# Kernel optimization log

Measured on AMD Instinct MI355X. Metric: run time of the kernel, lower is better.

The kernel has to match this reference:

```python
import jax, jax.numpy as jnp
import numpy as np

C = 512
H = 8

def setup_inputs() -> dict:
    key = jax.random.key(0)
    ks = jax.random.split(key, 5)
    x = jax.random.normal(ks[0], (4, C, 2048), dtype=jnp.float32)
    # Conv1d(kernel_size=1) == pointwise linear: weight [out, in], bias [out]
    qkv_w = jax.random.normal(ks[1], (3 * C, C), dtype=jnp.float32) * (1.0 / np.sqrt(C))
    qkv_b = jax.random.normal(ks[2], (3 * C,), dtype=jnp.float32) * 0.02
    proj_w = jax.random.normal(ks[3], (C, C), dtype=jnp.float32) * (1.0 / np.sqrt(C))
    proj_b = jax.random.normal(ks[4], (C,), dtype=jnp.float32) * 0.02
    return {"x": x, "qkv_w": qkv_w, "qkv_b": qkv_b, "proj_w": proj_w, "proj_b": proj_b}

def reference(x, qkv_w, qkv_b, proj_w, proj_b):
    b, c, t = x.shape
    scale = c ** (-0.5)  # NOTE: full channel count, matching the torch module
    # pointwise conv: [3C, C] @ [b, C, T] -> [b, 3C, T]
    qkv = jnp.einsum('oc,bct->bot', qkv_w, x) + qkv_b[None, :, None]
    q, k, v = jnp.split(qkv, 3, axis=1)
    d = c // H
    q = q.reshape(b, H, d, t)
    k = k.reshape(b, H, d, t)
    v = v.reshape(b, H, d, t)
    attn = jnp.einsum('bhct,bhcs->bhts', q, k) * scale
    attn = jax.nn.softmax(attn, axis=-1)
    out = jnp.einsum('bhts,bhcs->bhct', attn, v)
    out = out.reshape(b, c, t)
    out = jnp.einsum('oc,bct->bot', proj_w, out) + proj_b[None, :, None]
    return x + out
```

## Files before the change

### kernel.cpp

```cpp
#include <hip/hip_runtime.h>
#include <hip/hip_bf16.h>
#include <math.h>

#define B_DIM 4
#define C_DIM 512
#define T_DIM 2048
#define H_DIM 8
#define OC3   1536
#define VN_STRIDE 2064
#define SCALE 0.044194173824159216f
#define SCALE2 (0.044194173824159216f * 1.4426950408889634f)

typedef unsigned short ushortT;
typedef unsigned int uintT;
typedef __attribute__((ext_vector_type(8))) short bf16x8;
typedef __attribute__((ext_vector_type(4))) short bf16x4;
typedef __attribute__((ext_vector_type(4))) float f32x4;

__device__ __forceinline__ ushortT f2bf(float f) {
    union { float f; uintT u; } v; v.f = f;
    uintT r = v.u + 0x7FFF + ((v.u >> 16) & 1);
    return (ushortT)(r >> 16);
}
__device__ __forceinline__ float bf2f(ushortT h) {
    union { uintT u; float f; } v; v.u = ((uintT)h) << 16;
    return v.f;
}
__device__ __forceinline__ uintT pack2bf(float a, float b) {
    uintT ua = __float_as_uint(a) + 0x8000u;
    uintT ub = __float_as_uint(b) + 0x8000u;
    return (ua >> 16) | (ub & 0xFFFF0000u);
}
__device__ __forceinline__ uintT cvtpk2bf(float a, float b) {
    union { __bf16 v[2]; uintT u; } c;
    c.v[0] = (__bf16)a; c.v[1] = (__bf16)b;
    return c.u;
}
__device__ __forceinline__ void gload_lds16(const ushortT* g, ushortT* l) {
    __builtin_amdgcn_global_load_lds(
        (const __attribute__((address_space(1))) void*)g,
        (__attribute__((address_space(3))) void*)l, 16, 0, 0);
}

__global__ __launch_bounds__(256) void prep(const float* __restrict__ x,
                                            const float* __restrict__ qw,
                                            const float* __restrict__ pw,
                                            ushortT* __restrict__ xb,
                                            ushortT* __restrict__ qwb,
                                            ushortT* __restrict__ pwb) {
    __shared__ float xs[64][65];
    const int tid = threadIdx.x;
    const int blk = blockIdx.x;
    if (blk >= 1024) {
        int idx = ((blk - 1024) * 256 + tid) * 4;
        if (idx < OC3 * C_DIM) {
            float4 v = *(const float4*)(qw + idx);
            qwb[idx + 0] = f2bf(v.x); qwb[idx + 1] = f2bf(v.y);
            qwb[idx + 2] = f2bf(v.z); qwb[idx + 3] = f2bf(v.w);
        } else {
            idx -= OC3 * C_DIM;
            float4 v = *(const float4*)(pw + idx);
            pwb[idx + 0] = f2bf(v.x); pwb[idx + 1] = f2bf(v.y);
            pwb[idx + 2] = f2bf(v.z); pwb[idx + 3] = f2bf(v.w);
        }
        return;
    }
    const int b = blk >> 8, rem = blk & 255;
    const int c0 = (rem >> 5) * 64, t0 = (rem & 31) * 64;
    #pragma unroll
    for (int it = 0; it < 4; ++it) {
        int idx = it * 256 + tid;
        int r = idx >> 4, ch = idx & 15;
        float4 v = *(const float4*)(x + ((size_t)(b * C_DIM + c0 + r)) * T_DIM + t0 + ch * 4);
        xs[r][ch * 4 + 0] = v.x; xs[r][ch * 4 + 1] = v.y;
        xs[r][ch * 4 + 2] = v.z; xs[r][ch * 4 + 3] = v.w;
    }
    __syncthreads();
    #pragma unroll
    for (int it = 0; it < 2; ++it) {
        int idx = it * 256 + tid;
        int rt = idx >> 3, ch = idx & 7;
        union { ushortT s[8]; uint4 v; } tmp;
        #pragma unroll
        for (int k = 0; k < 8; ++k) tmp.s[k] = f2bf(xs[ch * 8 + k][rt]);
        *(uint4*)(xb + ((size_t)b * T_DIM + t0 + rt) * C_DIM + c0 + ch * 8) = tmp.v;
    }
}

__global__ __launch_bounds__(256, 2) void gemm_qkv(const ushortT* __restrict__ A,
                                                   const ushortT* __restrict__ Bw,
                                                   const float* __restrict__ bias,
                                                   ushortT* __restrict__ out,
                                                   ushortT* __restrict__ Vn) {
    __shared__ __align__(16) ushortT As[8192], Bs[8192];
    const int tid = threadIdx.x, lane = tid & 63, wid = tid >> 6;
    const int u = lane & 15, q = lane >> 4;
    const int wm = wid & 1, wn = wid >> 1;
    const int m0 = blockIdx.x * 128, n0 = blockIdx.y * 128;
    const int lrow = lane >> 2, lcol = (lane & 3) * 8;

    f32x4 acc[4][4];
    const f32x4 z = {0.f, 0.f, 0.f, 0.f};
    #pragma unroll
    for (int mi = 0; mi < 4; ++mi)
        #pragma unroll
        for (int ni = 0; ni < 4; ++ni) acc[mi][ni] = z;

    for (int k0 = 0; k0 < 512; k0 += 64) {
        __syncthreads();
        gload_lds16(A  + (size_t)(m0 + wid * 32 +      lrow) * 512 + k0      + lcol, &As[(wid * 32     ) * 32]);
        gload_lds16(A  + (size_t)(m0 + wid * 32 + 16 + lrow) * 512 + k0      + lcol, &As[(wid * 32 + 16) * 32]);
        gload_lds16(A  + (size_t)(m0 + wid * 32 +      lrow) * 512 + k0 + 32 + lcol, &As[4096 + (wid * 32     ) * 32]);
        gload_lds16(A  + (size_t)(m0 + wid * 32 + 16 + lrow) * 512 + k0 + 32 + lcol, &As[4096 + (wid * 32 + 16) * 32]);
        gload_lds16(Bw + (size_t)(n0 + wid * 32 +      lrow) * 512 + k0      + lcol, &Bs[(wid * 32     ) * 32]);
        gload_lds16(Bw + (size_t)(n0 + wid * 32 + 16 + lrow) * 512 + k0      + lcol, &Bs[(wid * 32 + 16) * 32]);
        gload_lds16(Bw + (size_t)(n0 + wid * 32 +      lrow) * 512 + k0 + 32 + lcol, &Bs[4096 + (wid * 32     ) * 32]);
        gload_lds16(Bw + (size_t)(n0 + wid * 32 + 16 + lrow) * 512 + k0 + 32 + lcol, &Bs[4096 + (wid * 32 + 16) * 32]);
        __syncthreads();
        bf16x8 af[4][2], bfr[4][2];
        #pragma unroll
        for (int mi = 0; mi < 4; ++mi) {
            af[mi][0] = *(const bf16x8*)&As[(wm * 64 + mi * 16 + u) * 32 + q * 8];
            af[mi][1] = *(const bf16x8*)&As[4096 + (wm * 64 + mi * 16 + u) * 32 + q * 8];
        }
        #pragma unroll
        for (int ni = 0; ni < 4; ++ni) {
            bfr[ni][0] = *(const bf16x8*)&Bs[(wn * 64 + ni * 16 + u) * 32 + q * 8];
            bfr[ni][1] = *(const bf16x8*)&Bs[4096 + (wn * 64 + ni * 16 + u) * 32 + q * 8];
        }
        #pragma unroll
        for (int mi = 0; mi < 4; ++mi)
            #pragma unroll
            for (int ni = 0; ni < 4; ++ni) {
                acc[mi][ni] = __builtin_amdgcn_mfma_f32_16x16x32_bf16(
                    af[mi][0], bfr[ni][0], acc[mi][ni], 0, 0, 0);
                acc[mi][ni] = __builtin_amdgcn_mfma_f32_16x16x32_bf16(
                    af[mi][1], bfr[ni][1], acc[mi][ni], 0, 0, 0);
            }
    }
    if (n0 < 1024) {
        const float scl = (n0 < 512) ? SCALE2 : 1.0f;
        #pragma unroll
        for (int ni = 0; ni < 4; ++ni) {
            int o = n0 + wn * 64 + ni * 16 + u;
            float bv = bias[o];
            #pragma unroll
            for (int mi = 0; mi < 4; ++mi)
                #pragma unroll
                for (int r = 0; r < 4; ++r) {
                    int m = m0 + wm * 64 + mi * 16 + q * 4 + r;
                    out[(size_t)m * OC3 + o] = f2bf((acc[mi][ni][r] + bv) * scl);
                }
        }
    } else {
        #pragma unroll
        for (int ni = 0; ni < 4; ++ni) {
            int o = n0 + wn * 64 + ni * 16 + u;
            float bv = bias[o];
            int oo = o - 1024;
            int hv = oo >> 6, d = oo & 63;
            #pragma unroll
            for (int mi = 0; mi < 4; ++mi) {
                int m = m0 + wm * 64 + mi * 16 + q * 4;
                int b = m >> 11, t = m & 2047;
                uint2 w;
                w.x = pack2bf(acc[mi][ni][0] + bv, acc[mi][ni][1] + bv);
                w.y = pack2bf(acc[mi][ni][2] + bv, acc[mi][ni][3] + bv);
                *(uint2*)(Vn + ((size_t)((b * 8 + hv) * 64 + d)) * VN_STRIDE + t) = w;
            }
        }
    }
}

__global__ __launch_bounds__(256, 2)
void flash(const ushortT* __restrict__ qkvT, const ushortT* __restrict__ Vn,
           ushortT* __restrict__ AO)
{
    __shared__ __align__(16) ushortT smem[16384];

    const int tid = threadIdx.x, lane = tid & 63, wid = tid >> 6;
    const int u = lane & 15, q = lane >> 4;
    const int g = blockIdx.x;
    const int bh = (g & 7) * 4 + ((g >> 3) & 3);
    const int qt = g >> 5;
    const int bb = bh >> 3, h = bh & 7;
    const int q0 = qt * 128;
    const size_t qbase = (size_t)bb * T_DIM * OC3;

    bf16x8 qb[2][2];
    #pragma unroll
    for (int ti = 0; ti < 2; ++ti)
        #pragma unroll
        for (int kst = 0; kst < 2; ++kst)
            qb[ti][kst] = *(const bf16x8*)(qkvT + qbase
                + (size_t)(q0 + wid * 32 + ti * 16 + u) * OC3 + h * 64 + kst * 32 + q * 8);

    const int rs = wid * 8 + (lane >> 3);
    const int sg = (lane & 7) ^ (rs & 7);
    const ushortT* ks0 = qkvT + qbase + (size_t)(rs     ) * OC3 + 512 + h * 64 + sg * 8;
    const ushortT* ks1 = qkvT + qbase + (size_t)(rs + 32) * OC3 + 512 + h * 64 + sg * 8;
    const ushortT* vs0 = Vn + ((size_t)bh * 64 + rs     ) * VN_STRIDE + sg * 8;
    const ushortT* vs1 = Vn + ((size_t)bh * 64 + rs + 32) * VN_STRIDE + sg * 8;

    f32x4 acc[4][2];
    const f32x4 z = {0.f, 0.f, 0.f, 0.f};
    #pragma unroll
    for (int ci = 0; ci < 4; ++ci)
        #pragma unroll
        for (int ti = 0; ti < 2; ++ti) acc[ci][ti] = z;
    f32x4 lacc[2] = {z, z};
    const bf16x4 ones = {(short)0x3F80, (short)0x3F80, (short)0x3F80, (short)0x3F80};

    gload_lds16(ks0, &smem[       wid * 512]);
    gload_lds16(ks1, &smem[2048 + wid * 512]);
    gload_lds16(vs0, &smem[8192 +        wid * 512]);
    gload_lds16(vs1, &smem[8192 + 2048 + wid * 512]);
    ks0 += 64 * OC3; ks1 += 64 * OC3; vs0 += 64; vs1 += 64;
    __syncthreads();

    int cur = 0;
    for (int rnd = 0; rnd < 32; ++rnd) {
        if (rnd < 31) {
            int nb = cur ^ 1;
            gload_lds16(ks0, &smem[nb * 4096 +        wid * 512]);
            gload_lds16(ks1, &smem[nb * 4096 + 2048 + wid * 512]);
            gload_lds16(vs0, &smem[8192 + nb * 4096 +        wid * 512]);
            gload_lds16(vs1, &smem[8192 + nb * 4096 + 2048 + wid * 512]);
            ks0 += 64 * OC3; ks1 += 64 * OC3; vs0 += 64; vs1 += 64;
        }
        const ushortT* Kb = &smem[cur * 4096];
        const ushortT* Vb = &smem[8192 + cur * 4096];
        bf16x8 ka[4][2];
        #pragma unroll
        for (int si = 0; si < 4; ++si)
            #pragma unroll
            for (int kst = 0; kst < 2; ++kst)
                ka[si][kst] = *(const bf16x8*)&Kb[(si * 16 + u) * 64
                    + (((kst * 4 + q) ^ (u & 7)) * 8)];
        bf16x4 va[4][4];
        #pragma unroll
        for (int si = 0; si < 4; ++si)
            #pragma unroll
            for (int ci = 0; ci < 4; ++ci)
                va[si][ci] = *(const bf16x4*)&Vb[(ci * 16 + u) * 64
                    + (((si * 2 + (q >> 1)) ^ (u & 7)) * 8) + (q & 1) * 4];

        #pragma unroll
        for (int si = 0; si < 4; ++si) {
            f32x4 sacc[2] = {z, z};
            #pragma unroll
            for (int ti = 0; ti < 2; ++ti)
                sacc[ti] = __builtin_amdgcn_mfma_f32_16x16x32_bf16(
                    ka[si][0], qb[ti][0], sacc[ti], 0, 0, 0);
            #pragma unroll
            for (int ti = 0; ti < 2; ++ti)
                sacc[ti] = __builtin_amdgcn_mfma_f32_16x16x32_bf16(
                    ka[si][1], qb[ti][1], sacc[ti], 0, 0, 0);
            #pragma unroll
            for (int ti = 0; ti < 2; ++ti) {
                float p0 = __builtin_amdgcn_exp2f(sacc[ti][0]);
                float p1 = __builtin_amdgcn_exp2f(sacc[ti][1]);
                float p2 = __builtin_amdgcn_exp2f(sacc[ti][2]);
                float p3 = __builtin_amdgcn_exp2f(sacc[ti][3]);
                union { uint2 u2; bf16x4 v; } pw;
                pw.u2.x = cvtpk2bf(p0, p1);
                pw.u2.y = cvtpk2bf(p2, p3);
                lacc[ti] = __builtin_amdgcn_mfma_f32_16x16x16bf16_1k(
                    ones, pw.v, lacc[ti], 0, 0, 0);
                #pragma unroll
                for (int ci = 0; ci < 4; ++ci)
                    acc[ci][ti] = __builtin_amdgcn_mfma_f32_16x16x16bf16_1k(
                        va[si][ci], pw.v, acc[ci][ti], 0, 0, 0);
            }
        }
        __syncthreads();
        cur ^= 1;
    }

    ushortT* Ob = smem + wid * 2304;
    float* Lb = (float*)(smem + 9216);
    if (q == 0) {
        Lb[wid * 32 + u]      = lacc[0][0];
        Lb[wid * 32 + 16 + u] = lacc[1][0];
    }
    #pragma unroll
    for (int ci = 0; ci < 4; ++ci)
        #pragma unroll
        for (int ti = 0; ti < 2; ++ti) {
            uint2 w;
            w.x = pack2bf(acc[ci][ti][0], acc[ci][ti][1]);
            w.y = pack2bf(acc[ci][ti][2], acc[ci][ti][3]);
            *(uint2*)&Ob[(ti * 16 + u) * 72 + ci * 16 + q * 4] = w;
        }
    __syncthreads();
    {
        const int row = tid >> 1, cs = (tid & 1) * 32;
        const int w = row >> 5, r32 = row & 31;
        float linv = 1.0f / Lb[w * 32 + r32];
        const ushortT* rp = smem + w * 2304 + r32 * 72 + cs;
        size_t orow = ((size_t)bb * T_DIM + q0 + row) * C_DIM + h * 64 + cs;
        #pragma unroll
        for (int j = 0; j < 4; ++j) {
            uint4 rv = *(const uint4*)(rp + j * 8);
            const uintT* rpp = (const uintT*)&rv;
            uint4 o;
            uintT* op = (uintT*)&o;
            #pragma unroll
            for (int k = 0; k < 4; ++k)
                op[k] = pack2bf(bf2f((ushortT)(rpp[k] & 0xFFFF)) * linv,
                                bf2f((ushortT)(rpp[k] >> 16)) * linv);
            *(uint4*)(AO + orow + j * 8) = o;
        }
    }
}

__global__ __launch_bounds__(256, 2) void gemm_proj(const ushortT* __restrict__ Wp,
                                                    const ushortT* __restrict__ AOv,
                                                    const float* __restrict__ bias,
                                                    const float* __restrict__ xres,
                                                    float* __restrict__ out) {
    __shared__ __align__(16) ushortT As[8192], Bs[8192];
    const int tid = threadIdx.x, lane = tid & 63, wid = tid >> 6;
    const int u = lane & 15, q = lane >> 4;
    const int wm = wid & 1, wn = wid >> 1;
    const int m0 = blockIdx.y * 128, n0 = blockIdx.x * 128;
    const int lrow = lane >> 2, lcol = (lane & 3) * 8;

    f32x4 acc[4][4];
    const f32x4 z = {0.f, 0.f, 0.f, 0.f};
    #pragma unroll
    for (int mi = 0; mi < 4; ++mi)
        #pragma unroll
        for (int ni = 0; ni < 4; ++ni) acc[mi][ni] = z;

    for (int k0 = 0; k0 < 512; k0 += 64) {
        __syncthreads();
        gload_lds16(Wp  + (size_t)(m0 + wid * 32 +      lrow) * 512 + k0      + lcol, &As[(wid * 32     ) * 32]);
        gload_lds16(Wp  + (size_t)(m0 + wid * 32 + 16 + lrow) * 512 + k0      + lcol, &As[(wid * 32 + 16) * 32]);
        gload_lds16(Wp  + (size_t)(m0 + wid * 32 +      lrow) * 512 + k0 + 32 + lcol, &As[4096 + (wid * 32     ) * 32]);
        gload_lds16(Wp  + (size_t)(m0 + wid * 32 + 16 + lrow) * 512 + k0 + 32 + lcol, &As[4096 + (wid * 32 + 16) * 32]);
        gload_lds16(AOv + (size_t)(n0 + wid * 32 +      lrow) * 512 + k0      + lcol, &Bs[(wid * 32     ) * 32]);
        gload_lds16(AOv + (size_t)(n0 + wid * 32 + 16 + lrow) * 512 + k0      + lcol, &Bs[(wid * 32 + 16) * 32]);
        gload_lds16(AOv + (size_t)(n0 + wid * 32 +      lrow) * 512 + k0 + 32 + lcol, &Bs[4096 + (wid * 32     ) * 32]);
        gload_lds16(AOv + (size_t)(n0 + wid * 32 + 16 + lrow) * 512 + k0 + 32 + lcol, &Bs[4096 + (wid * 32 + 16) * 32]);
        __syncthreads();
        bf16x8 af[4][2], bfr[4][2];
        #pragma unroll
        for (int mi = 0; mi < 4; ++mi) {
            af[mi][0] = *(const bf16x8*)&As[(wm * 64 + mi * 16 + u) * 32 + q * 8];
            af[mi][1] = *(const bf16x8*)&As[4096 + (wm * 64 + mi * 16 + u) * 32 + q * 8];
        }
        #pragma unroll
        for (int ni = 0; ni < 4; ++ni) {
            bfr[ni][0] = *(const bf16x8*)&Bs[(wn * 64 + ni * 16 + u) * 32 + q * 8];
            bfr[ni][1] = *(const bf16x8*)&Bs[4096 + (wn * 64 + ni * 16 + u) * 32 + q * 8];
        }
        #pragma unroll
        for (int mi = 0; mi < 4; ++mi)
            #pragma unroll
            for (int ni = 0; ni < 4; ++ni) {
                acc[mi][ni] = __builtin_amdgcn_mfma_f32_16x16x32_bf16(
                    af[mi][0], bfr[ni][0], acc[mi][ni], 0, 0, 0);
                acc[mi][ni] = __builtin_amdgcn_mfma_f32_16x16x32_bf16(
                    af[mi][1], bfr[ni][1], acc[mi][ni], 0, 0, 0);
            }
    }
    #pragma unroll
    for (int mi = 0; mi < 4; ++mi)
        #pragma unroll
        for (int r = 0; r < 4; ++r) {
            int o = m0 + wm * 64 + mi * 16 + q * 4 + r;
            float bv = bias[o];
            #pragma unroll
            for (int ni = 0; ni < 4; ++ni) {
                int n = n0 + wn * 64 + ni * 16 + u;
                int b = n >> 11, t = n & 2047;
                size_t oi = ((size_t)b * C_DIM + o) * T_DIM + t;
                out[oi] = acc[mi][ni][r] + bv + xres[oi];
            }
        }
}

extern "C" void kernel_launch(void* const* d_in, const int* in_sizes, int n_in,
                              void* d_out, int out_size, void* d_ws, size_t ws_size,
                              hipStream_t stream)
{
    const float* x      = (const float*)d_in[0];
    const float* qkv_w  = (const float*)d_in[1];
    const float* qkv_b  = (const float*)d_in[2];
    const float* proj_w = (const float*)d_in[3];
    const float* proj_b = (const float*)d_in[4];
    float* out = (float*)d_out;

    char* ws = (char*)d_ws;
    ushortT* xb   = (ushortT*)(ws);
    ushortT* wqb  = (ushortT*)(ws +  8388608);
    ushortT* wpb  = (ushortT*)(ws +  9961472);
    ushortT* qkvT = (ushortT*)(ws + 10485760);
    ushortT* Vn   = (ushortT*)(ws + 35651584);
    ushortT* AO   = (ushortT*)(ws + 44105728);

    prep     <<<2048, 256, 0, stream>>>(x, qkv_w, proj_w, xb, wqb, wpb);
    gemm_qkv <<<dim3(64, 12),   256, 0, stream>>>(xb, wqb, qkv_b, qkvT, Vn);
    flash    <<<512,            256, 0, stream>>>(qkvT, Vn, AO);
    gemm_proj<<<dim3(64, 4),    256, 0, stream>>>(wpb, AO, proj_b, x, out);
}
```

Measured before the change: 158.8 us.

## Halve flash attention query tile to 64 rows with 2-wave blocks

The flash kernel now uses 128-thread blocks of two waves, each covering 64 query rows, and launches 1024 blocks instead of 512. The K/V tile loading is reworked so each wave loads 32 rows in four chunks. The goal is more blocks for better CU occupancy and load balance across the GPU. The cost is that each K/V tile is reused by fewer query rows, so global K/V traffic per output doubles and each thread issues more loads. LDS usage per block stays the same.

```diff
diff --git a/kernel.cpp b/kernel.cpp
--- a/kernel.cpp
+++ b/kernel.cpp
@@ -172,7 +172,7 @@
     }
 }
 
-__global__ __launch_bounds__(256, 2)
+__global__ __launch_bounds__(128, 2)
 void flash(const ushortT* __restrict__ qkvT, const ushortT* __restrict__ Vn,
            ushortT* __restrict__ AO)
 {
@@ -184,7 +184,7 @@
     const int bh = (g & 7) * 4 + ((g >> 3) & 3);
     const int qt = g >> 5;
     const int bb = bh >> 3, h = bh & 7;
-    const int q0 = qt * 128;
+    const int q0 = qt * 64;
     const size_t qbase = (size_t)bb * T_DIM * OC3;
 
     bf16x8 qb[2][2];
@@ -195,12 +195,10 @@
             qb[ti][kst] = *(const bf16x8*)(qkvT + qbase
                 + (size_t)(q0 + wid * 32 + ti * 16 + u) * OC3 + h * 64 + kst * 32 + q * 8);
 
-    const int rs = wid * 8 + (lane >> 3);
-    const int sg = (lane & 7) ^ (rs & 7);
-    const ushortT* ks0 = qkvT + qbase + (size_t)(rs     ) * OC3 + 512 + h * 64 + sg * 8;
-    const ushortT* ks1 = qkvT + qbase + (size_t)(rs + 32) * OC3 + 512 + h * 64 + sg * 8;
-    const ushortT* vs0 = Vn + ((size_t)bh * 64 + rs     ) * VN_STRIDE + sg * 8;
-    const ushortT* vs1 = Vn + ((size_t)bh * 64 + rs + 32) * VN_STRIDE + sg * 8;
+    const int srow = wid * 32 + (lane >> 3);
+    const int sg = (lane & 7) ^ ((lane >> 3) & 7);
+    const ushortT* ksrc = qkvT + qbase + (size_t)srow * OC3 + 512 + h * 64 + sg * 8;
+    const ushortT* vsrc = Vn + ((size_t)bh * 64 + srow) * VN_STRIDE + sg * 8;
 
     f32x4 acc[4][2];
     const f32x4 z = {0.f, 0.f, 0.f, 0.f};
@@ -211,22 +209,24 @@
     f32x4 lacc[2] = {z, z};
     const bf16x4 ones = {(short)0x3F80, (short)0x3F80, (short)0x3F80, (short)0x3F80};
 
-    gload_lds16(ks0, &smem[       wid * 512]);
-    gload_lds16(ks1, &smem[2048 + wid * 512]);
-    gload_lds16(vs0, &smem[8192 +        wid * 512]);
-    gload_lds16(vs1, &smem[8192 + 2048 + wid * 512]);
-    ks0 += 64 * OC3; ks1 += 64 * OC3; vs0 += 64; vs1 += 64;
+    #pragma unroll
+    for (int c = 0; c < 4; ++c) {
+        gload_lds16(ksrc + (size_t)c * 8 * OC3,       &smem[       wid * 2048 + c * 512]);
+        gload_lds16(vsrc + (size_t)c * 8 * VN_STRIDE, &smem[8192 + wid * 2048 + c * 512]);
+    }
+    ksrc += 64 * OC3; vsrc += 64;
     __syncthreads();
 
     int cur = 0;
     for (int rnd = 0; rnd < 32; ++rnd) {
         if (rnd < 31) {
             int nb = cur ^ 1;
-            gload_lds16(ks0, &smem[nb * 4096 +        wid * 512]);
-            gload_lds16(ks1, &smem[nb * 4096 + 2048 + wid * 512]);
-            gload_lds16(vs0, &smem[8192 + nb * 4096 +        wid * 512]);
-            gload_lds16(vs1, &smem[8192 + nb * 4096 + 2048 + wid * 512]);
-            ks0 += 64 * OC3; ks1 += 64 * OC3; vs0 += 64; vs1 += 64;
+            #pragma unroll
+            for (int c = 0; c < 4; ++c) {
+                gload_lds16(ksrc + (size_t)c * 8 * OC3,       &smem[nb * 4096 +        wid * 2048 + c * 512]);
+                gload_lds16(vsrc + (size_t)c * 8 * VN_STRIDE, &smem[8192 + nb * 4096 + wid * 2048 + c * 512]);
+            }
+            ksrc += 64 * OC3; vsrc += 64;
         }
         const ushortT* Kb = &smem[cur * 4096];
         const ushortT* Vb = &smem[8192 + cur * 4096];
@@ -296,7 +296,7 @@
     {
         const int row = tid >> 1, cs = (tid & 1) * 32;
         const int w = row >> 5, r32 = row & 31;
-        float linv = 1.0f / Lb[w * 32 + r32];
+        float linv = 1.0f / Lb[row];
         const ushortT* rp = smem + w * 2304 + r32 * 72 + cs;
         size_t orow = ((size_t)bb * T_DIM + q0 + row) * C_DIM + h * 64 + cs;
         #pragma unroll
@@ -402,6 +402,6 @@
 
     prep     <<<2048, 256, 0, stream>>>(x, qkv_w, proj_w, xb, wqb, wpb);
     gemm_qkv <<<dim3(64, 12),   256, 0, stream>>>(xb, wqb, qkv_b, qkvT, Vn);
-    flash    <<<512,            256, 0, stream>>>(qkvT, Vn, AO);
+    flash    <<<1024,           128, 0, stream>>>(qkvT, Vn, AO);
     gemm_proj<<<dim3(64, 4),    256, 0, stream>>>(wpb, AO, proj_b, x, out);
 }
```

After: 161.4 us. Within noise of the previous version (+1.6%).

## Double-buffer LDS tiles in QKV and projection GEMMs to overlap loads

Applied to the files above, without the earlier changes.

Both pointwise GEMM kernels now use two shared-memory buffers. The next K-slice is issued via global-to-LDS loads while MFMAs run on the current slice, and the per-step barrier count drops from two to one. This is meant to hide global memory latency in the K loop. LDS use per block doubles to 64KB, which may limit occupancy. Correctness depends on the async loads being complete at the barrier.

```diff
diff --git a/kernel.cpp b/kernel.cpp
--- a/kernel.cpp
+++ b/kernel.cpp
@@ -92,13 +92,16 @@
                                                    const float* __restrict__ bias,
                                                    ushortT* __restrict__ out,
                                                    ushortT* __restrict__ Vn) {
-    __shared__ __align__(16) ushortT As[8192], Bs[8192];
+    __shared__ __align__(16) ushortT As[2][8192], Bs[2][8192];
     const int tid = threadIdx.x, lane = tid & 63, wid = tid >> 6;
     const int u = lane & 15, q = lane >> 4;
     const int wm = wid & 1, wn = wid >> 1;
     const int m0 = blockIdx.x * 128, n0 = blockIdx.y * 128;
     const int lrow = lane >> 2, lcol = (lane & 3) * 8;
 
+    const ushortT* Ap = A  + (size_t)(m0 + wid * 32 + lrow) * 512 + lcol;
+    const ushortT* Bp = Bw + (size_t)(n0 + wid * 32 + lrow) * 512 + lcol;
+
     f32x4 acc[4][4];
     const f32x4 z = {0.f, 0.f, 0.f, 0.f};
     #pragma unroll
@@ -106,27 +109,32 @@
         #pragma unroll
         for (int ni = 0; ni < 4; ++ni) acc[mi][ni] = z;
 
+    #define STAGE_QKV(nb, k0) do { \
+        gload_lds16(Ap + (k0),              &As[nb][(wid * 32     ) * 32]); \
+        gload_lds16(Ap + 8192 + (k0),       &As[nb][(wid * 32 + 16) * 32]); \
+        gload_lds16(Ap + (k0) + 32,         &As[nb][4096 + (wid * 32     ) * 32]); \
+        gload_lds16(Ap + 8192 + (k0) + 32,  &As[nb][4096 + (wid * 32 + 16) * 32]); \
+        gload_lds16(Bp + (k0),              &Bs[nb][(wid * 32     ) * 32]); \
+        gload_lds16(Bp + 8192 + (k0),       &Bs[nb][(wid * 32 + 16) * 32]); \
+        gload_lds16(Bp + (k0) + 32,         &Bs[nb][4096 + (wid * 32     ) * 32]); \
+        gload_lds16(Bp + 8192 + (k0) + 32,  &Bs[nb][4096 + (wid * 32 + 16) * 32]); \
+    } while (0)
+
+    STAGE_QKV(0, 0);
+    __syncthreads();
+    int cur = 0;
     for (int k0 = 0; k0 < 512; k0 += 64) {
-        __syncthreads();
-        gload_lds16(A  + (size_t)(m0 + wid * 32 +      lrow) * 512 + k0      + lcol, &As[(wid * 32     ) * 32]);
-        gload_lds16(A  + (size_t)(m0 + wid * 32 + 16 + lrow) * 512 + k0      + lcol, &As[(wid * 32 + 16) * 32]);
-        gload_lds16(A  + (size_t)(m0 + wid * 32 +      lrow) * 512 + k0 + 32 + lcol, &As[4096 + (wid * 32     ) * 32]);
-        gload_lds16(A  + (size_t)(m0 + wid * 32 + 16 + lrow) * 512 + k0 + 32 + lcol, &As[4096 + (wid * 32 + 16) * 32]);
-        gload_lds16(Bw + (size_t)(n0 + wid * 32 +      lrow) * 512 + k0      + lcol, &Bs[(wid * 32     ) * 32]);
-        gload_lds16(Bw + (size_t)(n0 + wid * 32 + 16 + lrow) * 512 + k0      + lcol, &Bs[(wid * 32 + 16) * 32]);
-        gload_lds16(Bw + (size_t)(n0 + wid * 32 +      lrow) * 512 + k0 + 32 + lcol, &Bs[4096 + (wid * 32     ) * 32]);
-        gload_lds16(Bw + (size_t)(n0 + wid * 32 + 16 + lrow) * 512 + k0 + 32 + lcol, &Bs[4096 + (wid * 32 + 16) * 32]);
-        __syncthreads();
+        if (k0 < 448) STAGE_QKV(cur ^ 1, k0 + 64);
         bf16x8 af[4][2], bfr[4][2];
         #pragma unroll
         for (int mi = 0; mi < 4; ++mi) {
-            af[mi][0] = *(const bf16x8*)&As[(wm * 64 + mi * 16 + u) * 32 + q * 8];
-            af[mi][1] = *(const bf16x8*)&As[4096 + (wm * 64 + mi * 16 + u) * 32 + q * 8];
+            af[mi][0] = *(const bf16x8*)&As[cur][(wm * 64 + mi * 16 + u) * 32 + q * 8];
+            af[mi][1] = *(const bf16x8*)&As[cur][4096 + (wm * 64 + mi * 16 + u) * 32 + q * 8];
         }
         #pragma unroll
         for (int ni = 0; ni < 4; ++ni) {
-            bfr[ni][0] = *(const bf16x8*)&Bs[(wn * 64 + ni * 16 + u) * 32 + q * 8];
-            bfr[ni][1] = *(const bf16x8*)&Bs[4096 + (wn * 64 + ni * 16 + u) * 32 + q * 8];
+            bfr[ni][0] = *(const bf16x8*)&Bs[cur][(wn * 64 + ni * 16 + u) * 32 + q * 8];
+            bfr[ni][1] = *(const bf16x8*)&Bs[cur][4096 + (wn * 64 + ni * 16 + u) * 32 + q * 8];
         }
         #pragma unroll
         for (int mi = 0; mi < 4; ++mi)
@@ -137,7 +145,11 @@
                 acc[mi][ni] = __builtin_amdgcn_mfma_f32_16x16x32_bf16(
                     af[mi][1], bfr[ni][1], acc[mi][ni], 0, 0, 0);
             }
-    }
+        __syncthreads();
+        cur ^= 1;
+    }
+    #undef STAGE_QKV
+
     if (n0 < 1024) {
         const float scl = (n0 < 512) ? SCALE2 : 1.0f;
         #pragma unroll
@@ -319,13 +331,16 @@
                                                     const float* __restrict__ bias,
                                                     const float* __restrict__ xres,
                                                     float* __restrict__ out) {
-    __shared__ __align__(16) ushortT As[8192], Bs[8192];
+    __shared__ __align__(16) ushortT As[2][8192], Bs[2][8192];
     const int tid = threadIdx.x, lane = tid & 63, wid = tid >> 6;
     const int u = lane & 15, q = lane >> 4;
     const int wm = wid & 1, wn = wid >> 1;
     const int m0 = blockIdx.y * 128, n0 = blockIdx.x * 128;
     const int lrow = lane >> 2, lcol = (lane & 3) * 8;
 
+    const ushortT* Ap = Wp  + (size_t)(m0 + wid * 32 + lrow) * 512 + lcol;
+    const ushortT* Bp = AOv + (size_t)(n0 + wid * 32 + lrow) * 512 + lcol;
+
     f32x4 acc[4][4];
     const f32x4 z = {0.f, 0.f, 0.f, 0.f};
     #pragma unroll
@@ -333,27 +348,32 @@
         #pragma unroll
         for (int ni = 0; ni < 4; ++ni) acc[mi][ni] = z;
 
+    #define STAGE_PROJ(nb, k0) do { \
+        gload_lds16(Ap + (k0),              &As[nb][(wid * 32     ) * 32]); \
+        gload_lds16(Ap + 8192 + (k0),       &As[nb][(wid * 32 + 16) * 32]); \
+        gload_lds16(Ap + (k0) + 32,         &As[nb][4096 + (wid * 32     ) * 32]); \
+        gload_lds16(Ap + 8192 + (k0) + 32,  &As[nb][4096 + (wid * 32 + 16) * 32]); \
+        gload_lds16(Bp + (k0),              &Bs[nb][(wid * 32     ) * 32]); \
+        gload_lds16(Bp + 8192 + (k0),       &Bs[nb][(wid * 32 + 16) * 32]); \
+        gload_lds16(Bp + (k0) + 32,         &Bs[nb][4096 + (wid * 32     ) * 32]); \
+        gload_lds16(Bp + 8192 + (k0) + 32,  &Bs[nb][4096 + (wid * 32 + 16) * 32]); \
+    } while (0)
+
+    STAGE_PROJ(0, 0);
+    __syncthreads();
+    int cur = 0;
     for (int k0 = 0; k0 < 512; k0 += 64) {
-        __syncthreads();
-        gload_lds16(Wp  + (size_t)(m0 + wid * 32 +      lrow) * 512 + k0      + lcol, &As[(wid * 32     ) * 32]);
-        gload_lds16(Wp  + (size_t)(m0 + wid * 32 + 16 + lrow) * 512 + k0      + lcol, &As[(wid * 32 + 16) * 32]);
-        gload_lds16(Wp  + (size_t)(m0 + wid * 32 +      lrow) * 512 + k0 + 32 + lcol, &As[4096 + (wid * 32     ) * 32]);
-        gload_lds16(Wp  + (size_t)(m0 + wid * 32 + 16 + lrow) * 512 + k0 + 32 + lcol, &As[4096 + (wid * 32 + 16) * 32]);
-        gload_lds16(AOv + (size_t)(n0 + wid * 32 +      lrow) * 512 + k0      + lcol, &Bs[(wid * 32     ) * 32]);
-        gload_lds16(AOv + (size_t)(n0 + wid * 32 + 16 + lrow) * 512 + k0      + lcol, &Bs[(wid * 32 + 16) * 32]);
-        gload_lds16(AOv + (size_t)(n0 + wid * 32 +      lrow) * 512 + k0 + 32 + lcol, &Bs[4096 + (wid * 32     ) * 32]);
-        gload_lds16(AOv + (size_t)(n0 + wid * 32 + 16 + lrow) * 512 + k0 + 32 + lcol, &Bs[4096 + (wid * 32 + 16) * 32]);
-        __syncthreads();
+        if (k0 < 448) STAGE_PROJ(cur ^ 1, k0 + 64);
         bf16x8 af[4][2], bfr[4][2];
         #pragma unroll
         for (int mi = 0; mi < 4; ++mi) {
-            af[mi][0] = *(const bf16x8*)&As[(wm * 64 + mi * 16 + u) * 32 + q * 8];
-            af[mi][1] = *(const bf16x8*)&As[4096 + (wm * 64 + mi * 16 + u) * 32 + q * 8];
+            af[mi][0] = *(const bf16x8*)&As[cur][(wm * 64 + mi * 16 + u) * 32 + q * 8];
+            af[mi][1] = *(const bf16x8*)&As[cur][4096 + (wm * 64 + mi * 16 + u) * 32 + q * 8];
         }
         #pragma unroll
         for (int ni = 0; ni < 4; ++ni) {
-            bfr[ni][0] = *(const bf16x8*)&Bs[(wn * 64 + ni * 16 + u) * 32 + q * 8];
-            bfr[ni][1] = *(const bf16x8*)&Bs[4096 + (wn * 64 + ni * 16 + u) * 32 + q * 8];
+            bfr[ni][0] = *(const bf16x8*)&Bs[cur][(wn * 64 + ni * 16 + u) * 32 + q * 8];
+            bfr[ni][1] = *(const bf16x8*)&Bs[cur][4096 + (wn * 64 + ni * 16 + u) * 32 + q * 8];
         }
         #pragma unroll
         for (int mi = 0; mi < 4; ++mi)
@@ -364,7 +384,11 @@
                 acc[mi][ni] = __builtin_amdgcn_mfma_f32_16x16x32_bf16(
                     af[mi][1], bfr[ni][1], acc[mi][ni], 0, 0, 0);
             }
-    }
+        __syncthreads();
+        cur ^= 1;
+    }
+    #undef STAGE_PROJ
+
     #pragma unroll
     for (int mi = 0; mi < 4; ++mi)
         #pragma unroll
```

Result: slower. 166.7 us (+5.0%).
